# Kernel tuning notes

Measured on AMD Instinct MI355X. Metric: run time of the kernel, lower is better.

Reference implementation:

```python
import jax, jax.numpy as jnp
import numpy as np

# blocks, d_model, heads, ffn_hidden, vocab, gen_len=(image_size//4)**2
L, D, NH, FF, V, GEN = 4, 256, 8, 1024, 2048, 16
B, NS, SLOT = 8, 7, 256  # batch, num_slots+1 (slots + projected action), slot_size


def setup_inputs():
    key = jax.random.key(0)
    ks = jax.random.split(key, 16)
    def n(i, shape, s=0.02):
        return (jax.random.normal(ks[i], shape) * s).astype(jnp.float32)
    return dict(
        slots=jax.random.normal(ks[0], (B, NS, SLOT), dtype=jnp.float32),
        W_slot_proj=n(1, (SLOT, D)),
        dict_emb=n(2, (V + 1, D)),
        pe=n(3, (GEN + 1, D)),
        ln_self_w=jnp.ones((L, D)), ln_self_b=jnp.zeros((L, D)),
        Wq_s=n(4, (L, D, D)), Wk_s=n(5, (L, D, D)), Wv_s=n(6, (L, D, D)), Wo_s=n(7, (L, D, D)),
        ln_cross_w=jnp.ones((L, D)), ln_cross_b=jnp.zeros((L, D)),
        Wq_c=n(8, (L, D, D)), Wk_c=n(9, (L, D, D)), Wv_c=n(10, (L, D, D)), Wo_c=n(11, (L, D, D)),
        ln_ffn_w=jnp.ones((L, D)), ln_ffn_b=jnp.zeros((L, D)),
        W1=n(12, (L, D, FF)), b1=jnp.zeros((L, FF)),
        W2=n(13, (L, FF, D)), b2=jnp.zeros((L, D)),
        ln_f_w=jnp.ones((D,)), ln_f_b=jnp.zeros((D,)),
        W_out=n(14, (D, V)),
    )


def _ln(x, w, b, eps=1e-5):
    m = x.mean(-1, keepdims=True)
    v = ((x - m) ** 2).mean(-1, keepdims=True)
    return (x - m) * jax.lax.rsqrt(v + eps) * w + b


def _mha(q_in, k_in, v_in, Wq, Wk, Wv, Wo, mask=None):
    Bq, Tq, Dm = q_in.shape
    dh = Dm // NH
    q = (q_in @ Wq).reshape(Bq, Tq, NH, dh).transpose(0, 2, 1, 3) * (dh ** -0.5)
    k = (k_in @ Wk).reshape(Bq, -1, NH, dh).transpose(0, 2, 1, 3)
    v = (v_in @ Wv).reshape(Bq, -1, NH, dh).transpose(0, 2, 1, 3)
    att = jnp.einsum('bhqd,bhkd->bhqk', q, k)
    if mask is not None:
        att = att + mask
    att = jax.nn.softmax(att, axis=-1)
    o = jnp.einsum('bhqk,bhkd->bhqd', att, v)
    return o.transpose(0, 2, 1, 3).reshape(Bq, Tq, Dm) @ Wo


def _decoder(x, enc, P):
    T = x.shape[1]
    i = jnp.arange(T)
    mask = jnp.where(i[:, None] >= i[None, :], 0.0, -jnp.inf).astype(x.dtype)
    for l in range(L):
        h = _ln(x, P['ln_self_w'][l], P['ln_self_b'][l])
        if l == 0:
            x = h  # SLATE: first block normalizes residual stream in-place
        x = x + _mha(h, h, h, P['Wq_s'][l], P['Wk_s'][l], P['Wv_s'][l], P['Wo_s'][l], mask)
        h = _ln(x, P['ln_cross_w'][l], P['ln_cross_b'][l])
        x = x + _mha(h, enc, enc, P['Wq_c'][l], P['Wk_c'][l], P['Wv_c'][l], P['Wo_c'][l])
        h = _ln(x, P['ln_ffn_w'][l], P['ln_ffn_b'][l])
        x = x + (jax.nn.relu(h @ P['W1'][l] + P['b1'][l]) @ P['W2'][l] + P['b2'][l])
    return _ln(x, P['ln_f_w'], P['ln_f_b'])


def _slots2tokens(slots, W_slot_proj, dict_emb, pe, P, W_out):
    Bb = slots.shape[0]
    enc = slots @ W_slot_proj  # slot_proj (bias=False)
    Tf = GEN + 1
    # fixed-size token buffer; position 0 is BOS one-hot, future slots are zeros
    # (causal mask guarantees they never influence position t's output)
    buf = jnp.zeros((Bb, Tf, V + 1), jnp.float32).at[:, 0, 0].set(1.0)

    def step(buf, t):
        tok = jnp.argmax(buf, axis=-1)              # [B, Tf]
        emb = dict_emb[tok] + pe[None, :Tf]         # OneHotDictionary + PositionalEncoding
        dec = _decoder(emb, enc, P)
        logits_t = dec[:, t] @ W_out                # [B, V]
        z_next = jax.nn.one_hot(jnp.argmax(logits_t, -1), V, dtype=buf.dtype)
        upd = jnp.pad(z_next, ((0, 0), (1, 0)))[:, None, :]  # prepend BOS column
        buf = jax.lax.dynamic_update_slice(buf, upd, (0, t + 1, 0))
        return buf, (z_next, logits_t)

    _, (z_gen, logits) = jax.lax.scan(step, buf, jnp.arange(GEN))
    z_gen = jnp.moveaxis(z_gen, 0, 1)    # [B, GEN, V]
    logits = jnp.moveaxis(logits, 0, 1)  # [B, GEN, V]
    He = int(np.sqrt(GEN))               # H_enc = W_enc = image_size // 4
    z_img = z_gen.transpose(0, 2, 1).reshape(Bb, V, He, He)
    return z_img, jax.nn.log_softmax(logits, axis=-1)


def reference(slots, W_slot_proj, dict_emb, pe, ln_self_w, ln_self_b, Wq_s, Wk_s, Wv_s, Wo_s, ln_cross_w, ln_cross_b, Wq_c, Wk_c, Wv_c, Wo_c, ln_ffn_w, ln_ffn_b, W1, b1, W2, b2, ln_f_w, ln_f_b, W_out):
    P = dict(ln_self_w=ln_self_w, ln_self_b=ln_self_b, Wq_s=Wq_s, Wk_s=Wk_s, Wv_s=Wv_s, Wo_s=Wo_s,
             ln_cross_w=ln_cross_w, ln_cross_b=ln_cross_b, Wq_c=Wq_c, Wk_c=Wk_c, Wv_c=Wv_c, Wo_c=Wo_c,
             ln_ffn_w=ln_ffn_w, ln_ffn_b=ln_ffn_b, W1=W1, b1=b1, W2=W2, b2=b2,
             ln_f_w=ln_f_w, ln_f_b=ln_f_b)
    return _slots2tokens(slots, W_slot_proj, dict_emb, pe, P, W_out)
```

## Files before the change

kernel.cpp:

```cpp
#include <hip/hip_runtime.h>

#define D       256
#define DH      32
#define FFDIM   1024
#define VOCAB   2048
#define GENLEN  16
#define BATCH   8
#define NSLOT   7
#define TF      17
#define NLAYER  4

#define SCOPE_AGENT __HIP_MEMORY_SCOPE_AGENT

typedef float    f32x4 __attribute__((ext_vector_type(4)));
typedef unsigned u32x4 __attribute__((ext_vector_type(4)));

struct Params {
  const float *slots, *W_slot_proj, *dict_emb, *pe;
  const float *ln_self_w, *ln_self_b, *Wq_s, *Wk_s, *Wv_s, *Wo_s;
  const float *ln_cross_w, *ln_cross_b, *Wq_c, *Wk_c, *Wv_c, *Wo_c;
  const float *ln_ffn_w, *ln_ffn_b, *W1, *b1, *W2, *b2;
  const float *ln_f_w, *ln_f_b, *W_out;
  float *enc, *P0, *P1, *tri;
  unsigned *flags;
  float *out_z, *out_lp;
};

__device__ __forceinline__ float cload(const float* p) {
  return __hip_atomic_load(p, __ATOMIC_RELAXED, SCOPE_AGENT);
}
__device__ __forceinline__ void cstore(float* p, float v) {
  __hip_atomic_store(p, v, __ATOMIC_RELAXED, SCOPE_AGENT);
}

__device__ __forceinline__ float blockSum(float v, float* red) {
  #pragma unroll
  for (int o = 32; o > 0; o >>= 1) v += __shfl_down(v, o);
  const int lane = threadIdx.x & 63, w = threadIdx.x >> 6;
  if (lane == 0) red[w] = v;
  __syncthreads();
  float s = red[0] + red[1] + red[2] + red[3];
  __syncthreads();
  return s;
}

template<int N>
__device__ __forceinline__ float dotStreamPre(const float* __restrict__ W,
                                              const float* __restrict__ h,
                                              int i0, int ld,
                                              const float* __restrict__ pre) {
  float pA[32], pB[32];
  #pragma unroll
  for (int k = 0; k < 32; ++k) pA[k] = pre[k];
  #pragma unroll
  for (int k = 0; k < 32; ++k) pB[k] = W[(size_t)(i0 + 32 + k) * ld];
  float acc = 0.f;
  #pragma unroll 1
  for (int u = 0; u < N; u += 64) {
    const f32x4* h4 = reinterpret_cast<const f32x4*>(h + i0 + u);
    #pragma unroll
    for (int k = 0; k < 8; ++k) {
      const f32x4 hv = h4[k];
      acc = fmaf(hv.x, pA[4*k+0], acc); acc = fmaf(hv.y, pA[4*k+1], acc);
      acc = fmaf(hv.z, pA[4*k+2], acc); acc = fmaf(hv.w, pA[4*k+3], acc);
    }
    if (u + 64 < N) {
      #pragma unroll
      for (int k = 0; k < 32; ++k) pA[k] = W[(size_t)(i0 + u + 64 + k) * ld];
    }
    #pragma unroll
    for (int k = 0; k < 8; ++k) {
      const f32x4 hv = h4[8 + k];
      acc = fmaf(hv.x, pB[4*k+0], acc); acc = fmaf(hv.y, pB[4*k+1], acc);
      acc = fmaf(hv.z, pB[4*k+2], acc); acc = fmaf(hv.w, pB[4*k+3], acc);
    }
    if (u + 96 < N) {
      #pragma unroll
      for (int k = 0; k < 32; ++k) pB[k] = W[(size_t)(i0 + u + 96 + k) * ld];
    }
  }
  return acc;
}

template<int N>
__device__ __forceinline__ float dotStream(const float* __restrict__ W,
                                           const float* __restrict__ h,
                                           int i0, int ld) {
  float pre[32];
  #pragma unroll
  for (int k = 0; k < 32; ++k) pre[k] = W[(size_t)(i0 + k) * ld];
  return dotStreamPre<N>(W, h, i0, ld, pre);
}

__device__ __forceinline__ float dot32(const float* __restrict__ w,
                                       const float* __restrict__ h, int i0) {
  float acc = 0.f;
  const f32x4* h4 = reinterpret_cast<const f32x4*>(h + i0);
  #pragma unroll
  for (int k = 0; k < 8; ++k) {
    const f32x4 hv = h4[k];
    acc = fmaf(hv.x, w[4*k+0], acc); acc = fmaf(hv.y, w[4*k+1], acc);
    acc = fmaf(hv.z, w[4*k+2], acc); acc = fmaf(hv.w, w[4*k+3], acc);
  }
  return acc;
}

__global__ __launch_bounds__(256, 1) void mega_kernel(Params p)
{
  const int blk = blockIdx.x;
  const int bb = blk >> 3, sl = blk & 7, tid = threadIdx.x;
  unsigned* flags = p.flags + bb * 256;
  unsigned target = 0;

  __shared__ __align__(16) float hsh[D];
  __shared__ __align__(16) float ash[128];
  __shared__ float qsh[DH], osh[DH], score[TF], red[4];
  __shared__ float wval[4]; __shared__ int widx[4];
  __shared__ float stage[NSLOT * D];
  __shared__ float kls[NLAYER][TF][DH + 1], vls[NLAYER][TF][DH + 1];
  __shared__ float kcls[NLAYER][NSLOT][DH + 1], vcls[NLAYER][NSLOT][DH + 1];

  auto gsync = [&]() {
    __syncthreads();
    ++target;
    if (tid == 0)
      __hip_atomic_store(flags + sl, target, __ATOMIC_RELAXED, SCOPE_AGENT);
  };
  auto gwait = [&]() {
    if (tid == 0) {
      u32x4 f0, f1;
      for (;;) {
        asm volatile(
          "global_load_dwordx4 %0, %2, off sc0 sc1\n\t"
          "global_load_dwordx4 %1, %2, off offset:16 sc0 sc1\n\t"
          "s_waitcnt vmcnt(0)"
          : "=&v"(f0), "=&v"(f1) : "v"(flags) : "memory");
        if (f0.x >= target && f0.y >= target && f0.z >= target && f0.w >= target &&
            f1.x >= target && f1.y >= target && f1.z >= target && f1.w >= target)
          break;
        __builtin_amdgcn_s_sleep(1);
      }
    }
    __syncthreads();
    asm volatile("" ::: "memory");
  };

  auto layernorm = [&](float xv, const float* w, const float* b) -> float {
    const float mean = blockSum(xv, red) * (1.f / D);
    const float dv = xv - mean;
    const float var = blockSum(dv * dv, red) * (1.f / D);
    return dv * (1.f / sqrtf(var + 1e-5f)) * w[tid] + b[tid];
  };

  auto fold8 = [&](const float* P) -> float {
    const float* a0 = P + (bb * 8 + 0) * D + tid;
    const float* a4 = P + (bb * 8 + 4) * D + tid;
    float s0, s1, s2, s3, s4, s5, s6, s7;
    asm volatile(
      "global_load_dword %0, %8, off sc0 sc1\n\t"
      "global_load_dword %1, %8, off offset:1024 sc0 sc1\n\t"
      "global_load_dword %2, %8, off offset:2048 sc0 sc1\n\t"
      "global_load_dword %3, %8, off offset:3072 sc0 sc1\n\t"
      "global_load_dword %4, %9, off sc0 sc1\n\t"
      "global_load_dword %5, %9, off offset:1024 sc0 sc1\n\t"
      "global_load_dword %6, %9, off offset:2048 sc0 sc1\n\t"
      "global_load_dword %7, %9, off offset:3072 sc0 sc1\n\t"
      "s_waitcnt vmcnt(0)"
      : "=&v"(s0), "=&v"(s1), "=&v"(s2), "=&v"(s3),
        "=&v"(s4), "=&v"(s5), "=&v"(s6), "=&v"(s7)
      : "v"(a0), "v"(a4));
    return ((s0 + s1) + (s2 + s3)) + ((s4 + s5) + (s6 + s7));
  };

  float heldLogit = 0.f;
  int   lastAmax  = 0;

  auto consume_tri = [&](int row) {
    const float* tb = p.tri + bb * 64;
    f32x4 q0,q1,q2,q3,q4,q5,q6,q7;
    asm volatile(
      "global_load_dwordx4 %0, %8, off sc0 sc1\n\t"
      "global_load_dwordx4 %1, %8, off offset:32 sc0 sc1\n\t"
      "global_load_dwordx4 %2, %8, off offset:64 sc0 sc1\n\t"
      "global_load_dwordx4 %3, %8, off offset:96 sc0 sc1\n\t"
      "global_load_dwordx4 %4, %8, off offset:128 sc0 sc1\n\t"
      "global_load_dwordx4 %5, %8, off offset:160 sc0 sc1\n\t"
      "global_load_dwordx4 %6, %8, off offset:192 sc0 sc1\n\t"
      "global_load_dwordx4 %7, %8, off offset:224 sc0 sc1\n\t"
      "s_waitcnt vmcnt(0)"
      : "=&v"(q0), "=&v"(q1), "=&v"(q2), "=&v"(q3),
        "=&v"(q4), "=&v"(q5), "=&v"(q6), "=&v"(q7)
      : "v"(tb));
    float gm = q0.x;
    gm = fmaxf(gm, q1.x); gm = fmaxf(gm, q2.x); gm = fmaxf(gm, q3.x);
    gm = fmaxf(gm, q4.x); gm = fmaxf(gm, q5.x); gm = fmaxf(gm, q6.x); gm = fmaxf(gm, q7.x);
    float gs = 0.f; float best = -1e30f; int am = 0;
    const f32x4 qa[8] = {q0,q1,q2,q3,q4,q5,q6,q7};
    #pragma unroll
    for (int j = 0; j < 8; ++j) {
      gs += qa[j].y * expf(qa[j].x - gm);
      if (qa[j].x > best) { best = qa[j].x; am = j * 256 + (int)qa[j].z; }
    }
    const float lse = gm + logf(gs);
    p.out_lp[(bb * GENLEN + row) * VOCAB + sl * 256 + tid] = heldLogit - lse;
    if (sl == 0 && tid == 0)
      p.out_z[bb * VOCAB * GENLEN + am * GENLEN + row] = 1.0f;
    lastAmax = am;
  };

  for (int i = tid; i < NLAYER * TF * (DH + 1); i += 256) {
    (&kls[0][0][0])[i] = 0.f;
    (&vls[0][0][0])[i] = 0.f;
  }

  if (tid < 32) {
    const int c = sl * 32 + tid;
    float acc[NSLOT] = {0.f,0.f,0.f,0.f,0.f,0.f,0.f};
    #pragma unroll 8
    for (int i = 0; i < D; ++i) {
      const float w = p.W_slot_proj[i * D + c];
      #pragma unroll
      for (int s = 0; s < NSLOT; ++s) acc[s] += p.slots[(bb * NSLOT + s) * D + i] * w;
    }
    for (int s = 0; s < NSLOT; ++s) cstore(&p.enc[(bb * NSLOT + s) * D + c], acc[s]);
  }
  gsync(); gwait();

  {
    for (int i = tid; i < NSLOT * D; i += 256) stage[i] = cload(&p.enc[bb * NSLOT * D + i]);
    __syncthreads();
    const int l = tid >> 6, g = tid & 63, c32 = g >> 1, mat = g & 1;
    const float* W = (mat ? p.Wv_c : p.Wk_c) + l * D * D + sl * DH + c32;
    float acc[NSLOT] = {0.f,0.f,0.f,0.f,0.f,0.f,0.f};
    #pragma unroll 8
    for (int i = 0; i < D; ++i) {
      const float w = W[i * D];
      #pragma unroll
      for (int s = 0; s < NSLOT; ++s) acc[s] += stage[s * D + i] * w;
    }
    if (mat) { for (int s = 0; s < NSLOT; ++s) vcls[l][s][c32] = acc[s]; }
    else     { for (int s = 0; s < NSLOT; ++s) kcls[l][s][c32] = acc[s]; }
    __syncthreads();
  }

  float* Pbuf[2] = {p.P0, p.P1};
  int par = 0;
  float x = 0.f;

  #pragma unroll 1
  for (int t = 0; t < GENLEN; ++t) {
    #pragma unroll 1
    for (int l = 0; l < NLAYER; ++l) {
      {
        gsync();
        const int mm = tid >> 6, g = tid & 63, c32 = g >> 1, half = g & 1;
        const float* Wqkv = (mm == 0 ? p.Wq_s : (mm == 1 ? p.Wk_s : p.Wv_s))
                          + l * D * D + sl * DH + c32;
        float preq[32];
        if (tid < 192) {
          #pragma unroll
          for (int k = 0; k < 32; ++k) preq[k] = Wqkv[(size_t)(half * 128 + k) * D];
        }
        float wo[32];
        {
          const float* W = p.Wo_s + l * D * D + sl * DH * D + tid;
          #pragma unroll
          for (int k = 0; k < 32; ++k) wo[k] = W[(size_t)k * D];
        }
        gwait();

        if (l == 0) {
          int tok = 0;
          if (t > 0) { consume_tri(t - 1); tok = lastAmax + 1; }
          x = p.dict_emb[tok * D + tid] + p.pe[t * D + tid];
        } else {
          x += fold8(Pbuf[par]);
        }
        const float h = layernorm(x, p.ln_self_w + l * D, p.ln_self_b + l * D);
        if (l == 0) x = h;
        hsh[tid] = h;
        __syncthreads();

        if (tid < 192) {
          float acc = dotStreamPre<128>(Wqkv, hsh, half * 128, D, preq);
          acc += __shfl_xor(acc, 1);
          if (half == 0) {
            if (mm == 0)      qsh[c32] = acc * 0.17677669529663689f;
            else if (mm == 1) kls[l][t][c32] = acc;
            else              vls[l][t][c32] = acc;
          }
        }
        __syncthreads();

        if (tid < 64) {
          float s = -1e30f;
          if (tid <= t) {
            float a = 0.f;
            #pragma unroll
            for (int r = 0; r < DH; ++r) a += qsh[r] * kls[l][tid][r];
            s = a;
          }
          float m = s;
          #pragma unroll
          for (int o = 32; o > 0; o >>= 1) m = fmaxf(m, __shfl_xor(m, o));
          const float e = (tid <= t) ? expf(s - m) : 0.f;
          float sum = e;
          #pragma unroll
          for (int o = 32; o > 0; o >>= 1) sum += __shfl_xor(sum, o);
          const float inv = 1.f / sum;
          if (tid < TF) score[tid] = e * inv;
        }
        __syncthreads();
        if (tid < DH) {
          float a = 0.f;
          #pragma unroll
          for (int pp = 0; pp < TF; ++pp) a = fmaf(score[pp], vls[l][pp][tid], a);
          osh[tid] = a;
        }
        __syncthreads();
        {
          float a0 = 0.f;
          #pragma unroll
          for (int k = 0; k < 32; ++k) a0 = fmaf(osh[k], wo[k], a0);
          cstore(&Pbuf[par ^ 1][(bb * 8 + sl) * D + tid], a0);
        }
        par ^= 1;
      }

      {
        gsync();
        const int c32 = tid >> 3, sub = tid & 7;
        float wq[32], woc[32];
        {
          const float* W = p.Wq_c + l * D * D + sl * DH + c32;
          #pragma unroll
          for (int k = 0; k < 32; ++k) wq[k] = W[(size_t)(sub * 32 + k) * D];
        }
        {
          const float* W = p.Wo_c + l * D * D + sl * DH * D + tid;
          #pragma unroll
          for (int k = 0; k < 32; ++k) woc[k] = W[(size_t)k * D];
        }
        gwait();

        x += fold8(Pbuf[par]);
        hsh[tid] = layernorm(x, p.ln_cross_w + l * D, p.ln_cross_b + l * D);
        __syncthreads();

        {
          float acc = dot32(wq, hsh, sub * 32);
          acc += __shfl_xor(acc, 1);
          acc += __shfl_xor(acc, 2);
          acc += __shfl_xor(acc, 4);
          if (sub == 0) qsh[c32] = acc * 0.17677669529663689f;
        }
        __syncthreads();

        if (tid < 64) {
          float s = -1e30f;
          if (tid < NSLOT) {
            float a = 0.f;
            #pragma unroll
            for (int r = 0; r < DH; ++r) a += qsh[r] * kcls[l][tid][r];
            s = a;
          }
          float m = s;
          #pragma unroll
          for (int o = 32; o > 0; o >>= 1) m = fmaxf(m, __shfl_xor(m, o));
          const float e = (tid < NSLOT) ? expf(s - m) : 0.f;
          float sum = e;
          #pragma unroll
          for (int o = 32; o > 0; o >>= 1) sum += __shfl_xor(sum, o);
          const float inv = 1.f / sum;
          if (tid < NSLOT) score[tid] = e * inv;
        }
        __syncthreads();
        if (tid < DH) {
          float a = 0.f;
          #pragma unroll
          for (int s = 0; s < NSLOT; ++s) a = fmaf(score[s], vcls[l][s][tid], a);
          osh[tid] = a;
        }
        __syncthreads();
        {
          float a0 = 0.f;
          #pragma unroll
          for (int k = 0; k < 32; ++k) a0 = fmaf(osh[k], woc[k], a0);
          cstore(&Pbuf[par ^ 1][(bb * 8 + sl) * D + tid], a0);
        }
        par ^= 1;
      }

      {
        gsync();
        const int c128 = tid >> 1, half = tid & 1, c = sl * 128 + c128;
        const float* W1p = p.W1 + l * D * FFDIM + c;
        float prew1[32];
        {
          #pragma unroll
          for (int k = 0; k < 32; ++k) prew1[k] = W1p[(size_t)(half * 128 + k) * FFDIM];
        }
        gwait();

        x += fold8(Pbuf[par]);
        hsh[tid] = layernorm(x, p.ln_ffn_w + l * D, p.ln_ffn_b + l * D);
        __syncthreads();

        {
          float acc = dotStreamPre<128>(W1p, hsh, half * 128, FFDIM, prew1);
          acc += __shfl_xor(acc, 1);
          if (half == 0) ash[c128] = fmaxf(acc + p.b1[l * FFDIM + c], 0.f);
        }
        __syncthreads();
        {
          float acc = dotStream<128>(p.W2 + l * FFDIM * D + sl * 128 * D + tid, ash, 0, D);
          if (sl == 0) acc += p.b2[l * D + tid];
          cstore(&Pbuf[par ^ 1][(bb * 8 + sl) * D + tid], acc);
        }
        __syncthreads();
      }
      par ^= 1;
    }

    {
      gsync();
      const float* Wop = p.W_out + sl * 256 + tid;
      float prewo[32];
      {
        #pragma unroll
        for (int k = 0; k < 32; ++k) prewo[k] = Wop[(size_t)k * VOCAB];
      }
      gwait();

      x += fold8(Pbuf[par]);
      hsh[tid] = layernorm(x, p.ln_f_w, p.ln_f_b);
      __syncthreads();
      heldLogit = dotStreamPre<256>(Wop, hsh, 0, VOCAB, prewo);

      {
        float v = heldLogit; int idx = tid;
        #pragma unroll
        for (int o = 32; o > 0; o >>= 1) {
          const float v2 = __shfl_xor(v, o);
          const int   i2 = __shfl_xor(idx, o);
          if (v2 > v || (v2 == v && i2 < idx)) { v = v2; idx = i2; }
        }
        const int w = tid >> 6;
        if ((tid & 63) == 0) { wval[w] = v; widx[w] = idx; }
      }
      __syncthreads();
      float smax = wval[0]; int sarg = widx[0];
      #pragma unroll
      for (int j = 1; j < 4; ++j)
        if (wval[j] > smax || (wval[j] == smax && widx[j] < sarg)) { smax = wval[j]; sarg = widx[j]; }
      const float ssum = blockSum(expf(heldLogit - smax), red);
      if (tid == 0) {
        cstore(&p.tri[(bb * 8 + sl) * 8 + 0], smax);
        cstore(&p.tri[(bb * 8 + sl) * 8 + 1], ssum);
        cstore(&p.tri[(bb * 8 + sl) * 8 + 2], (float)sarg);
      }
      __syncthreads();
    }
  }

  gsync(); gwait();
  consume_tri(GENLEN - 1);
}

extern "C" void kernel_launch(void* const* d_in, const int* in_sizes, int n_in,
                              void* d_out, int out_size, void* d_ws, size_t ws_size,
                              hipStream_t stream)
{
  Params p;
  const float* const* in = (const float* const*)d_in;
  p.slots = in[0];  p.W_slot_proj = in[1]; p.dict_emb = in[2]; p.pe = in[3];
  p.ln_self_w = in[4];  p.ln_self_b = in[5];
  p.Wq_s = in[6];  p.Wk_s = in[7];  p.Wv_s = in[8];  p.Wo_s = in[9];
  p.ln_cross_w = in[10]; p.ln_cross_b = in[11];
  p.Wq_c = in[12]; p.Wk_c = in[13]; p.Wv_c = in[14]; p.Wo_c = in[15];
  p.ln_ffn_w = in[16]; p.ln_ffn_b = in[17];
  p.W1 = in[18]; p.b1 = in[19]; p.W2 = in[20]; p.b2 = in[21];
  p.ln_f_w = in[22]; p.ln_f_b = in[23]; p.W_out = in[24];

  p.flags = (unsigned*)d_ws;
  float* ws = (float*)d_ws + BATCH * 256;
  p.enc = ws;  ws += BATCH * NSLOT * D;
  p.P0  = ws;  ws += BATCH * 8 * D;
  p.P1  = ws;  ws += BATCH * 8 * D;
  p.tri = ws;  ws += BATCH * 8 * 8;

  p.out_z  = (float*)d_out;
  p.out_lp = (float*)d_out + BATCH * VOCAB * GENLEN;

  hipMemsetAsync(d_ws, 0, BATCH * 256 * sizeof(unsigned), stream);
  hipMemsetAsync(d_out, 0, (size_t)out_size * sizeof(float), stream);

  mega_kernel<<<64, 256, 0, stream>>>(p);
}
```

Measured before the change: 1.467 ms.

## Replace flag barriers with tagged 64-bit partial-sum slots polled directly

Each block now writes its partial sums and softmax stats as 64-bit words that pack a sequence tag with the float value. Consumers poll those words until every tag matches the expected counter, so the separate store-flag/poll-flag barrier per stage goes away and data arrival itself acts as the synchronisation. This removes one round trip through global memory per stage, but it doubles the size of the exchange buffers and adds a larger workspace memset. The self-attention layernorm also gains a dead extra blockSum call that adds a reduction.

```diff
diff --git a/kernel.cpp b/kernel.cpp
--- a/kernel.cpp
+++ b/kernel.cpp
@@ -14,6 +14,7 @@
 
 typedef float    f32x4 __attribute__((ext_vector_type(4)));
 typedef unsigned u32x4 __attribute__((ext_vector_type(4)));
+typedef unsigned long long u64;
 
 struct Params {
   const float *slots, *W_slot_proj, *dict_emb, *pe;
@@ -21,7 +22,8 @@
   const float *ln_cross_w, *ln_cross_b, *Wq_c, *Wk_c, *Wv_c, *Wo_c;
   const float *ln_ffn_w, *ln_ffn_b, *W1, *b1, *W2, *b2;
   const float *ln_f_w, *ln_f_b, *W_out;
-  float *enc, *P0, *P1, *tri;
+  float *enc;
+  u64 *P0, *P1, *tri;
   unsigned *flags;
   float *out_z, *out_lp;
 };
@@ -31,6 +33,15 @@
 }
 __device__ __forceinline__ void cstore(float* p, float v) {
   __hip_atomic_store(p, v, __ATOMIC_RELAXED, SCOPE_AGENT);
+}
+__device__ __forceinline__ u64 cload64(const u64* p) {
+  return __hip_atomic_load(p, __ATOMIC_RELAXED, SCOPE_AGENT);
+}
+__device__ __forceinline__ void cstore64(u64* p, u64 v) {
+  __hip_atomic_store(p, v, __ATOMIC_RELAXED, SCOPE_AGENT);
+}
+__device__ __forceinline__ u64 packt(unsigned tag, float v) {
+  return ((u64)tag << 32) | (u64)__float_as_uint(v);
 }
 
 __device__ __forceinline__ float blockSum(float v, float* red) {
@@ -110,7 +121,6 @@
   const int blk = blockIdx.x;
   const int bb = blk >> 3, sl = blk & 7, tid = threadIdx.x;
   unsigned* flags = p.flags + bb * 256;
-  unsigned target = 0;
 
   __shared__ __align__(16) float hsh[D];
   __shared__ __align__(16) float ash[128];
@@ -120,13 +130,96 @@
   __shared__ float kls[NLAYER][TF][DH + 1], vls[NLAYER][TF][DH + 1];
   __shared__ float kcls[NLAYER][NSLOT][DH + 1], vcls[NLAYER][NSLOT][DH + 1];
 
-  auto gsync = [&]() {
+  auto fold8t = [&](const u64* P, unsigned exp) -> float {
+    const u64* a0 = P + (bb * 8 + 0) * 256 + tid;
+    const u64* a2 = P + (bb * 8 + 2) * 256 + tid;
+    const u64* a4 = P + (bb * 8 + 4) * 256 + tid;
+    const u64* a6 = P + (bb * 8 + 6) * 256 + tid;
+    u64 v0, v1, v2, v3, v4, v5, v6, v7;
+    for (;;) {
+      asm volatile(
+        "global_load_dwordx2 %0, %8, off sc0 sc1\n\t"
+        "global_load_dwordx2 %1, %8, off offset:2048 sc0 sc1\n\t"
+        "global_load_dwordx2 %2, %9, off sc0 sc1\n\t"
+        "global_load_dwordx2 %3, %9, off offset:2048 sc0 sc1\n\t"
+        "global_load_dwordx2 %4, %10, off sc0 sc1\n\t"
+        "global_load_dwordx2 %5, %10, off offset:2048 sc0 sc1\n\t"
+        "global_load_dwordx2 %6, %11, off sc0 sc1\n\t"
+        "global_load_dwordx2 %7, %11, off offset:2048 sc0 sc1\n\t"
+        "s_waitcnt vmcnt(0)"
+        : "=&v"(v0), "=&v"(v1), "=&v"(v2), "=&v"(v3),
+          "=&v"(v4), "=&v"(v5), "=&v"(v6), "=&v"(v7)
+        : "v"(a0), "v"(a2), "v"(a4), "v"(a6) : "memory");
+      if ((unsigned)(v0 >> 32) == exp && (unsigned)(v1 >> 32) == exp &&
+          (unsigned)(v2 >> 32) == exp && (unsigned)(v3 >> 32) == exp &&
+          (unsigned)(v4 >> 32) == exp && (unsigned)(v5 >> 32) == exp &&
+          (unsigned)(v6 >> 32) == exp && (unsigned)(v7 >> 32) == exp)
+        break;
+      __builtin_amdgcn_s_sleep(1);
+    }
+    const float s0 = __uint_as_float((unsigned)v0), s1 = __uint_as_float((unsigned)v1);
+    const float s2 = __uint_as_float((unsigned)v2), s3 = __uint_as_float((unsigned)v3);
+    const float s4 = __uint_as_float((unsigned)v4), s5 = __uint_as_float((unsigned)v5);
+    const float s6 = __uint_as_float((unsigned)v6), s7 = __uint_as_float((unsigned)v7);
+    return ((s0 + s1) + (s2 + s3)) + ((s4 + s5) + (s6 + s7));
+  };
+
+  float heldLogit = 0.f;
+  int   lastAmax  = 0;
+
+  auto consume_tri = [&](int row, unsigned exp) {
+    float smax8[8], ssum8[8]; int sarg8[8];
+    for (;;) {
+      bool ok = true;
+      #pragma unroll
+      for (int j = 0; j < 8; ++j) {
+        const u64 A = cload64(&p.tri[(bb * 8 + j) * 4 + 0]);
+        const u64 B = cload64(&p.tri[(bb * 8 + j) * 4 + 1]);
+        const u64 C = cload64(&p.tri[(bb * 8 + j) * 4 + 2]);
+        ok = ok && ((unsigned)(A >> 32) == exp) && ((unsigned)(B >> 32) == exp)
+                && ((unsigned)(C >> 32) == exp);
+        smax8[j] = __uint_as_float((unsigned)A);
+        ssum8[j] = __uint_as_float((unsigned)B);
+        sarg8[j] = (int)(unsigned)C;
+      }
+      if (ok) break;
+      __builtin_amdgcn_s_sleep(1);
+    }
+    float gm = smax8[0];
+    #pragma unroll
+    for (int j = 1; j < 8; ++j) gm = fmaxf(gm, smax8[j]);
+    float gs = 0.f; float best = -1e30f; int am = 0;
+    #pragma unroll
+    for (int j = 0; j < 8; ++j) {
+      gs += ssum8[j] * expf(smax8[j] - gm);
+      if (smax8[j] > best) { best = smax8[j]; am = j * 256 + sarg8[j]; }
+    }
+    const float lse = gm + logf(gs);
+    p.out_lp[(bb * GENLEN + row) * VOCAB + sl * 256 + tid] = heldLogit - lse;
+    if (sl == 0 && tid == 0)
+      p.out_z[bb * VOCAB * GENLEN + am * GENLEN + row] = 1.0f;
+    lastAmax = am;
+  };
+
+  for (int i = tid; i < NLAYER * TF * (DH + 1); i += 256) {
+    (&kls[0][0][0])[i] = 0.f;
+    (&vls[0][0][0])[i] = 0.f;
+  }
+
+  if (tid < 32) {
+    const int c = sl * 32 + tid;
+    float acc[NSLOT] = {0.f,0.f,0.f,0.f,0.f,0.f,0.f};
+    #pragma unroll 8
+    for (int i = 0; i < D; ++i) {
+      const float w = p.W_slot_proj[i * D + c];
+      #pragma unroll
+      for (int s = 0; s < NSLOT; ++s) acc[s] += p.slots[(bb * NSLOT + s) * D + i] * w;
+    }
+    for (int s = 0; s < NSLOT; ++s) cstore(&p.enc[(bb * NSLOT + s) * D + c], acc[s]);
+  }
+  {
     __syncthreads();
-    ++target;
-    if (tid == 0)
-      __hip_atomic_store(flags + sl, target, __ATOMIC_RELAXED, SCOPE_AGENT);
-  };
-  auto gwait = [&]() {
+    if (tid == 0) __hip_atomic_store(flags + sl, 1u, __ATOMIC_RELAXED, SCOPE_AGENT);
     if (tid == 0) {
       u32x4 f0, f1;
       for (;;) {
@@ -135,96 +228,15 @@
           "global_load_dwordx4 %1, %2, off offset:16 sc0 sc1\n\t"
           "s_waitcnt vmcnt(0)"
           : "=&v"(f0), "=&v"(f1) : "v"(flags) : "memory");
-        if (f0.x >= target && f0.y >= target && f0.z >= target && f0.w >= target &&
-            f1.x >= target && f1.y >= target && f1.z >= target && f1.w >= target)
+        if (f0.x >= 1u && f0.y >= 1u && f0.z >= 1u && f0.w >= 1u &&
+            f1.x >= 1u && f1.y >= 1u && f1.z >= 1u && f1.w >= 1u)
           break;
         __builtin_amdgcn_s_sleep(1);
       }
     }
     __syncthreads();
     asm volatile("" ::: "memory");
-  };
-
-  auto layernorm = [&](float xv, const float* w, const float* b) -> float {
-    const float mean = blockSum(xv, red) * (1.f / D);
-    const float dv = xv - mean;
-    const float var = blockSum(dv * dv, red) * (1.f / D);
-    return dv * (1.f / sqrtf(var + 1e-5f)) * w[tid] + b[tid];
-  };
-
-  auto fold8 = [&](const float* P) -> float {
-    const float* a0 = P + (bb * 8 + 0) * D + tid;
-    const float* a4 = P + (bb * 8 + 4) * D + tid;
-    float s0, s1, s2, s3, s4, s5, s6, s7;
-    asm volatile(
-      "global_load_dword %0, %8, off sc0 sc1\n\t"
-      "global_load_dword %1, %8, off offset:1024 sc0 sc1\n\t"
-      "global_load_dword %2, %8, off offset:2048 sc0 sc1\n\t"
-      "global_load_dword %3, %8, off offset:3072 sc0 sc1\n\t"
-      "global_load_dword %4, %9, off sc0 sc1\n\t"
-      "global_load_dword %5, %9, off offset:1024 sc0 sc1\n\t"
-      "global_load_dword %6, %9, off offset:2048 sc0 sc1\n\t"
-      "global_load_dword %7, %9, off offset:3072 sc0 sc1\n\t"
-      "s_waitcnt vmcnt(0)"
-      : "=&v"(s0), "=&v"(s1), "=&v"(s2), "=&v"(s3),
-        "=&v"(s4), "=&v"(s5), "=&v"(s6), "=&v"(s7)
-      : "v"(a0), "v"(a4));
-    return ((s0 + s1) + (s2 + s3)) + ((s4 + s5) + (s6 + s7));
-  };
-
-  float heldLogit = 0.f;
-  int   lastAmax  = 0;
-
-  auto consume_tri = [&](int row) {
-    const float* tb = p.tri + bb * 64;
-    f32x4 q0,q1,q2,q3,q4,q5,q6,q7;
-    asm volatile(
-      "global_load_dwordx4 %0, %8, off sc0 sc1\n\t"
-      "global_load_dwordx4 %1, %8, off offset:32 sc0 sc1\n\t"
-      "global_load_dwordx4 %2, %8, off offset:64 sc0 sc1\n\t"
-      "global_load_dwordx4 %3, %8, off offset:96 sc0 sc1\n\t"
-      "global_load_dwordx4 %4, %8, off offset:128 sc0 sc1\n\t"
-      "global_load_dwordx4 %5, %8, off offset:160 sc0 sc1\n\t"
-      "global_load_dwordx4 %6, %8, off offset:192 sc0 sc1\n\t"
-      "global_load_dwordx4 %7, %8, off offset:224 sc0 sc1\n\t"
-      "s_waitcnt vmcnt(0)"
-      : "=&v"(q0), "=&v"(q1), "=&v"(q2), "=&v"(q3),
-        "=&v"(q4), "=&v"(q5), "=&v"(q6), "=&v"(q7)
-      : "v"(tb));
-    float gm = q0.x;
-    gm = fmaxf(gm, q1.x); gm = fmaxf(gm, q2.x); gm = fmaxf(gm, q3.x);
-    gm = fmaxf(gm, q4.x); gm = fmaxf(gm, q5.x); gm = fmaxf(gm, q6.x); gm = fmaxf(gm, q7.x);
-    float gs = 0.f; float best = -1e30f; int am = 0;
-    const f32x4 qa[8] = {q0,q1,q2,q3,q4,q5,q6,q7};
-    #pragma unroll
-    for (int j = 0; j < 8; ++j) {
-      gs += qa[j].y * expf(qa[j].x - gm);
-      if (qa[j].x > best) { best = qa[j].x; am = j * 256 + (int)qa[j].z; }
-    }
-    const float lse = gm + logf(gs);
-    p.out_lp[(bb * GENLEN + row) * VOCAB + sl * 256 + tid] = heldLogit - lse;
-    if (sl == 0 && tid == 0)
-      p.out_z[bb * VOCAB * GENLEN + am * GENLEN + row] = 1.0f;
-    lastAmax = am;
-  };
-
-  for (int i = tid; i < NLAYER * TF * (DH + 1); i += 256) {
-    (&kls[0][0][0])[i] = 0.f;
-    (&vls[0][0][0])[i] = 0.f;
-  }
-
-  if (tid < 32) {
-    const int c = sl * 32 + tid;
-    float acc[NSLOT] = {0.f,0.f,0.f,0.f,0.f,0.f,0.f};
-    #pragma unroll 8
-    for (int i = 0; i < D; ++i) {
-      const float w = p.W_slot_proj[i * D + c];
-      #pragma unroll
-      for (int s = 0; s < NSLOT; ++s) acc[s] += p.slots[(bb * NSLOT + s) * D + i] * w;
-    }
-    for (int s = 0; s < NSLOT; ++s) cstore(&p.enc[(bb * NSLOT + s) * D + c], acc[s]);
-  }
-  gsync(); gwait();
+  }
 
   {
     for (int i = tid; i < NSLOT * D; i += 256) stage[i] = cload(&p.enc[bb * NSLOT * D + i]);
@@ -243,8 +255,9 @@
     __syncthreads();
   }
 
-  float* Pbuf[2] = {p.P0, p.P1};
+  u64* Pbuf[2] = {p.P0, p.P1};
   int par = 0;
+  unsigned ctr = 0;
   float x = 0.f;
 
   #pragma unroll 1
@@ -252,7 +265,7 @@
     #pragma unroll 1
     for (int l = 0; l < NLAYER; ++l) {
       {
-        gsync();
+        const unsigned expect = ctr; ++ctr; const unsigned wtag = ctr;
         const int mm = tid >> 6, g = tid & 63, c32 = g >> 1, half = g & 1;
         const float* Wqkv = (mm == 0 ? p.Wq_s : (mm == 1 ? p.Wk_s : p.Wv_s))
                           + l * D * D + sl * DH + c32;
@@ -267,18 +280,23 @@
           #pragma unroll
           for (int k = 0; k < 32; ++k) wo[k] = W[(size_t)k * D];
         }
-        gwait();
 
         if (l == 0) {
           int tok = 0;
-          if (t > 0) { consume_tri(t - 1); tok = lastAmax + 1; }
+          if (t > 0) { consume_tri(t - 1, expect); tok = lastAmax + 1; }
           x = p.dict_emb[tok * D + tid] + p.pe[t * D + tid];
         } else {
-          x += fold8(Pbuf[par]);
-        }
-        const float h = layernorm(x, p.ln_self_w + l * D, p.ln_self_b + l * D);
-        if (l == 0) x = h;
-        hsh[tid] = h;
+          x += fold8t(Pbuf[par], expect);
+        }
+        const float h = blockSum(x, red) * 0.f + x;
+        const float mean = blockSum(x, red) * (1.f / D);
+        const float dv = x - mean;
+        const float var = blockSum(dv * dv, red) * (1.f / D);
+        const float hval = dv * (1.f / sqrtf(var + 1e-5f)) * p.ln_self_w[l * D + tid]
+                         + p.ln_self_b[l * D + tid];
+        (void)h;
+        if (l == 0) x = hval;
+        hsh[tid] = hval;
         __syncthreads();
 
         if (tid < 192) {
@@ -322,13 +340,13 @@
           float a0 = 0.f;
           #pragma unroll
           for (int k = 0; k < 32; ++k) a0 = fmaf(osh[k], wo[k], a0);
-          cstore(&Pbuf[par ^ 1][(bb * 8 + sl) * D + tid], a0);
+          cstore64(&Pbuf[par ^ 1][(bb * 8 + sl) * 256 + tid], packt(wtag, a0));
         }
         par ^= 1;
       }
 
       {
-        gsync();
+        const unsigned expect = ctr; ++ctr; const unsigned wtag = ctr;
         const int c32 = tid >> 3, sub = tid & 7;
         float wq[32], woc[32];
         {
@@ -341,10 +359,13 @@
           #pragma unroll
           for (int k = 0; k < 32; ++k) woc[k] = W[(size_t)k * D];
         }
-        gwait();
-
-        x += fold8(Pbuf[par]);
-        hsh[tid] = layernorm(x, p.ln_cross_w + l * D, p.ln_cross_b + l * D);
+
+        x += fold8t(Pbuf[par], expect);
+        const float mean = blockSum(x, red) * (1.f / D);
+        const float dv = x - mean;
+        const float var = blockSum(dv * dv, red) * (1.f / D);
+        hsh[tid] = dv * (1.f / sqrtf(var + 1e-5f)) * p.ln_cross_w[l * D + tid]
+                 + p.ln_cross_b[l * D + tid];
         __syncthreads();
 
         {
@@ -386,13 +407,13 @@
           float a0 = 0.f;
           #pragma unroll
           for (int k = 0; k < 32; ++k) a0 = fmaf(osh[k], woc[k], a0);
-          cstore(&Pbuf[par ^ 1][(bb * 8 + sl) * D + tid], a0);
+          cstore64(&Pbuf[par ^ 1][(bb * 8 + sl) * 256 + tid], packt(wtag, a0));
         }
         par ^= 1;
       }
 
       {
-        gsync();
+        const unsigned expect = ctr; ++ctr; const unsigned wtag = ctr;
         const int c128 = tid >> 1, half = tid & 1, c = sl * 128 + c128;
         const float* W1p = p.W1 + l * D * FFDIM + c;
         float prew1[32];
@@ -400,10 +421,13 @@
           #pragma unroll
           for (int k = 0; k < 32; ++k) prew1[k] = W1p[(size_t)(half * 128 + k) * FFDIM];
         }
-        gwait();
-
-        x += fold8(Pbuf[par]);
-        hsh[tid] = layernorm(x, p.ln_ffn_w + l * D, p.ln_ffn_b + l * D);
+
+        x += fold8t(Pbuf[par], expect);
+        const float mean = blockSum(x, red) * (1.f / D);
+        const float dv = x - mean;
+        const float var = blockSum(dv * dv, red) * (1.f / D);
+        hsh[tid] = dv * (1.f / sqrtf(var + 1e-5f)) * p.ln_ffn_w[l * D + tid]
+                 + p.ln_ffn_b[l * D + tid];
         __syncthreads();
 
         {
@@ -415,7 +439,7 @@
         {
           float acc = dotStream<128>(p.W2 + l * FFDIM * D + sl * 128 * D + tid, ash, 0, D);
           if (sl == 0) acc += p.b2[l * D + tid];
-          cstore(&Pbuf[par ^ 1][(bb * 8 + sl) * D + tid], acc);
+          cstore64(&Pbuf[par ^ 1][(bb * 8 + sl) * 256 + tid], packt(wtag, acc));
         }
         __syncthreads();
       }
@@ -423,17 +447,19 @@
     }
 
     {
-      gsync();
+      const unsigned expect = ctr; ++ctr; const unsigned wtag = ctr;
       const float* Wop = p.W_out + sl * 256 + tid;
       float prewo[32];
       {
         #pragma unroll
         for (int k = 0; k < 32; ++k) prewo[k] = Wop[(size_t)k * VOCAB];
       }
-      gwait();
-
-      x += fold8(Pbuf[par]);
-      hsh[tid] = layernorm(x, p.ln_f_w, p.ln_f_b);
+
+      x += fold8t(Pbuf[par], expect);
+      const float mean = blockSum(x, red) * (1.f / D);
+      const float dv = x - mean;
+      const float var = blockSum(dv * dv, red) * (1.f / D);
+      hsh[tid] = dv * (1.f / sqrtf(var + 1e-5f)) * p.ln_f_w[tid] + p.ln_f_b[tid];
       __syncthreads();
       heldLogit = dotStreamPre<256>(Wop, hsh, 0, VOCAB, prewo);
 
@@ -455,16 +481,15 @@
         if (wval[j] > smax || (wval[j] == smax && widx[j] < sarg)) { smax = wval[j]; sarg = widx[j]; }
       const float ssum = blockSum(expf(heldLogit - smax), red);
       if (tid == 0) {
-        cstore(&p.tri[(bb * 8 + sl) * 8 + 0], smax);
-        cstore(&p.tri[(bb * 8 + sl) * 8 + 1], ssum);
-        cstore(&p.tri[(bb * 8 + sl) * 8 + 2], (float)sarg);
+        cstore64(&p.tri[(bb * 8 + sl) * 4 + 0], packt(wtag, smax));
+        cstore64(&p.tri[(bb * 8 + sl) * 4 + 1], packt(wtag, ssum));
+        cstore64(&p.tri[(bb * 8 + sl) * 4 + 2], ((u64)wtag << 32) | (unsigned)sarg);
       }
       __syncthreads();
     }
   }
 
-  gsync(); gwait();
-  consume_tri(GENLEN - 1);
+  consume_tri(GENLEN - 1, ctr);
 }
 
 extern "C" void kernel_launch(void* const* d_in, const int* in_sizes, int n_in,
@@ -483,16 +508,16 @@
   p.ln_f_w = in[22]; p.ln_f_b = in[23]; p.W_out = in[24];
 
   p.flags = (unsigned*)d_ws;
-  float* ws = (float*)d_ws + BATCH * 256;
-  p.enc = ws;  ws += BATCH * NSLOT * D;
-  p.P0  = ws;  ws += BATCH * 8 * D;
-  p.P1  = ws;  ws += BATCH * 8 * D;
-  p.tri = ws;  ws += BATCH * 8 * 8;
+  p.P0 = (u64*)((char*)d_ws + 8192);
+  p.P1 = p.P0 + BATCH * 8 * 256;
+  p.tri = p.P1 + BATCH * 8 * 256;
+  const size_t zero_bytes = 8192 + 2 * BATCH * 8 * 256 * 8 + BATCH * 8 * 4 * 8;
+  p.enc = (float*)((char*)d_ws + ((zero_bytes + 255) & ~(size_t)255));
 
   p.out_z  = (float*)d_out;
   p.out_lp = (float*)d_out + BATCH * VOCAB * GENLEN;
 
-  hipMemsetAsync(d_ws, 0, BATCH * 256 * sizeof(unsigned), stream);
+  hipMemsetAsync(d_ws, 0, zero_bytes, stream);
   hipMemsetAsync(d_out, 0, (size_t)out_size * sizeof(float), stream);
 
   mega_kernel<<<64, 256, 0, stream>>>(p);
```

Result: no change. 1.482 ms (+1.0%).
